# Optimization experiments

Hardware: AMD Instinct MI355X
Metric: run time of the kernel (lower is better)

Reference implementation:

```python
import jax, jax.numpy as jnp
import numpy as np
import math

HEAD_DIM = 128
N_HEADS_Q = 32
N_KV_HEADS = 8
N_REP = N_HEADS_Q // N_KV_HEADS
ROPE_BASE = 10000.0


def _rope(x, start_pos):
    # x: [b, s, h, d] -- rotate interleaved pairs, Llama-style
    b, s, h, d = x.shape
    pos = start_pos + jnp.arange(s, dtype=jnp.float32)            # [s]
    inv_freq = 1.0 / (ROPE_BASE ** (jnp.arange(0, d, 2, dtype=jnp.float32) / d))  # [d/2]
    ang = pos[:, None] * inv_freq[None, :]                         # [s, d/2]
    cos = jnp.cos(ang)[None, :, None, :].astype(x.dtype)
    sin = jnp.sin(ang)[None, :, None, :].astype(x.dtype)
    x1 = x[..., 0::2]
    x2 = x[..., 1::2]
    out = jnp.stack([x1 * cos - x2 * sin, x1 * sin + x2 * cos], axis=-1)
    return out.reshape(b, s, h, d)


def setup_inputs() -> dict:
    key = jax.random.key(0)
    ks = jax.random.split(key, 5)
    dim = N_HEADS_Q * HEAD_DIM
    kv_dim = N_KV_HEADS * HEAD_DIM
    sc = 0.02
    return {
        "x": jax.random.normal(ks[0], (2, 2048, dim), dtype=jnp.float32),
        "wq": jax.random.normal(ks[1], (dim, dim), dtype=jnp.float32) * sc,
        "wk": jax.random.normal(ks[2], (kv_dim, dim), dtype=jnp.float32) * sc,
        "wv": jax.random.normal(ks[3], (kv_dim, dim), dtype=jnp.float32) * sc,
        "wo": jax.random.normal(ks[4], (dim, dim), dtype=jnp.float32) * sc,
        "start_pos": 0,
    }


def reference(x, wq, wk, wv, wo, start_pos):
    b, s, dim = x.shape
    # QKV projections (nn.Linear: y = x @ W.T)
    xq = (x @ wq.T).reshape(b, s, N_HEADS_Q, HEAD_DIM)
    xk = (x @ wk.T).reshape(b, s, N_KV_HEADS, HEAD_DIM)
    xv = (x @ wv.T).reshape(b, s, N_KV_HEADS, HEAD_DIM)
    xq = _rope(xq, start_pos)
    xk = _rope(xk, start_pos)
    # KV cache: start_pos=0 prefill -> cached prefix == freshly written xk/xv
    keys, values = xk, xv
    # GQA attention without materializing repeated KV:
    # q grouped as [b, q, n_kv, n_rep, d]
    qg = xq.reshape(b, s, N_KV_HEADS, N_REP, HEAD_DIM)
    scores = jnp.einsum("bqhrd,bkhd->bhrqk", qg, keys) / math.sqrt(HEAD_DIM)
    probs = jax.nn.softmax(scores, axis=-1)  # no causal mask in original
    out = jnp.einsum("bhrqk,bkhd->bqhrd", probs, values)
    out = out.reshape(b, s, N_HEADS_Q * HEAD_DIM)
    return out @ wo.T
```

## Files before the change

kernel.cpp:

```cpp
#include <hip/hip_runtime.h>
#include <cstdint>
#include <cstddef>

typedef _Float16 f16x8 __attribute__((ext_vector_type(8)));
typedef _Float16 f16x4 __attribute__((ext_vector_type(4)));
typedef _Float16 f16x2 __attribute__((ext_vector_type(2)));
typedef float    f32x4 __attribute__((ext_vector_type(4)));
typedef uint32_t u32x4 __attribute__((ext_vector_type(4)));

__device__ __forceinline__ void async16(const void* g, void* l) {
  __builtin_amdgcn_global_load_lds(
      (const __attribute__((address_space(1))) void*)g,
      (__attribute__((address_space(3))) void*)l, 16, 0, 0);
}

__global__ void cvt5_kernel(const float* __restrict__ s0, const float* __restrict__ s1,
                            const float* __restrict__ s2, const float* __restrict__ s3,
                            const float* __restrict__ s4,
                            _Float16* __restrict__ d0, _Float16* __restrict__ d1,
                            _Float16* __restrict__ d2, _Float16* __restrict__ d3,
                            _Float16* __restrict__ d4,
                            int n0, int n1, int n2, int n3, int n4c) {
  const float* src; _Float16* dst; int n4;
  switch (blockIdx.y) {
    case 0:  src = s0; dst = d0; n4 = n0;  break;
    case 1:  src = s1; dst = d1; n4 = n1;  break;
    case 2:  src = s2; dst = d2; n4 = n2;  break;
    case 3:  src = s3; dst = d3; n4 = n3;  break;
    default: src = s4; dst = d4; n4 = n4c; break;
  }
  int i = blockIdx.x * blockDim.x + threadIdx.x;
  int stride = gridDim.x * blockDim.x;
  for (; i < n4; i += stride) {
    float4 f = ((const float4*)src)[i];
    f16x4 o;
    o[0] = (_Float16)f.x; o[1] = (_Float16)f.y;
    o[2] = (_Float16)f.z; o[3] = (_Float16)f.w;
    ((f16x4*)dst)[i] = o;
  }
}

__global__ void rope2_kernel(_Float16* __restrict__ XQ, _Float16* __restrict__ XK,
                             const int* __restrict__ sp, int sMask,
                             int nPairsQ, int nPairsK) {
  _Float16* X; int ppShift, nPairs;
  if (blockIdx.y == 0) { X = XQ; ppShift = 11; nPairs = nPairsQ; }
  else                 { X = XK; ppShift = 9;  nPairs = nPairsK; }
  int i = blockIdx.x * blockDim.x + threadIdx.x;
  int stride = gridDim.x * blockDim.x;
  int start = *sp;
  for (int p = i; p < nPairs; p += stride) {
    int row = p >> ppShift;
    int pc  = p & ((1 << ppShift) - 1);
    int fi  = pc & 63;
    int s   = row & sMask;
    float ang = (float)(start + s) * exp2f(-0.20762050593046014f * (float)fi);
    float sn, cs;
    __sincosf(ang, &sn, &cs);
    uint32_t u = ((uint32_t*)X)[p];
    f16x2 v = __builtin_bit_cast(f16x2, u);
    float x1 = (float)v[0], x2 = (float)v[1];
    v[0] = (_Float16)(x1 * cs - x2 * sn);
    v[1] = (_Float16)(x1 * sn + x2 * cs);
    ((uint32_t*)X)[p] = __builtin_bit_cast(uint32_t, v);
  }
}

template<int OUT_MODE>
__global__ __launch_bounds__(256, 3)
void gemm_nt(const _Float16* __restrict__ A, const _Float16* __restrict__ B,
             void* __restrict__ Cp, void* __restrict__ Cp2, void* __restrict__ Cp3,
             int M, int N, int K) {
  __shared__ __align__(16) _Float16 As[128 * 64];
  __shared__ __align__(16) _Float16 Bs[128 * 64];
  const int tid  = threadIdx.x;
  const int wave = tid >> 6, lane = tid & 63;
  const int l15  = lane & 15, quad = lane >> 4;
  const int m0 = blockIdx.y * 128, n0 = blockIdx.x * 128;
  const int wm = (wave >> 1) * 64, wn = (wave & 1) * 64;
  f32x4 acc[4][4] = {};
  const int cbase = wave * 256;

  for (int kb = 0; kb < K; kb += 64) {
    #pragma unroll
    for (int i = 0; i < 4; ++i) {
      int base = cbase + i * 64;
      int idx  = base + lane;
      int row  = idx >> 3, pos = idx & 7;
      int c    = pos ^ (row & 7);
      async16(A + (size_t)(m0 + row) * K + kb + c * 8, (char*)As + base * 16);
      async16(B + (size_t)(n0 + row) * K + kb + c * 8, (char*)Bs + base * 16);
    }
    __syncthreads();
    #pragma unroll
    for (int ks = 0; ks < 2; ++ks) {
      f16x8 af[4], bfv[4];
      #pragma unroll
      for (int t = 0; t < 4; ++t) {
        int ra = wm + t * 16 + l15;
        int pa = (ks * 4 + quad) ^ (ra & 7);
        af[t] = *(const f16x8*)((const char*)As + ra * 128 + pa * 16);
        int rb = wn + t * 16 + l15;
        int pb = (ks * 4 + quad) ^ (rb & 7);
        bfv[t] = *(const f16x8*)((const char*)Bs + rb * 128 + pb * 16);
      }
      #pragma unroll
      for (int mt = 0; mt < 4; ++mt)
        #pragma unroll
        for (int nt = 0; nt < 4; ++nt)
          acc[mt][nt] = __builtin_amdgcn_mfma_f32_16x16x32_f16(af[mt], bfv[nt], acc[mt][nt], 0, 0, 0);
    }
    __syncthreads();
  }

  if constexpr (OUT_MODE == 2) {
    float* Cf = (float*)Cp;
    #pragma unroll
    for (int mt = 0; mt < 4; ++mt)
      #pragma unroll
      for (int r = 0; r < 4; ++r) {
        size_t row = (size_t)(m0 + wm + mt * 16 + quad * 4 + r);
        #pragma unroll
        for (int nt = 0; nt < 4; ++nt)
          Cf[row * N + n0 + wn + nt * 16 + l15] = acc[mt][nt][r];
      }
  } else if constexpr (OUT_MODE == 4) {
    if (n0 < 4096) {
      _Float16* Cb = (_Float16*)Cp;
      #pragma unroll
      for (int mt = 0; mt < 4; ++mt)
        #pragma unroll
        for (int r = 0; r < 4; ++r) {
          size_t row = (size_t)(m0 + wm + mt * 16 + quad * 4 + r);
          #pragma unroll
          for (int nt = 0; nt < 4; ++nt)
            Cb[row * 4096 + n0 + wn + nt * 16 + l15] = (_Float16)acc[mt][nt][r];
        }
    } else if (n0 < 5120) {
      _Float16* Cb = (_Float16*)Cp2;
      #pragma unroll
      for (int mt = 0; mt < 4; ++mt)
        #pragma unroll
        for (int r = 0; r < 4; ++r) {
          size_t row = (size_t)(m0 + wm + mt * 16 + quad * 4 + r);
          #pragma unroll
          for (int nt = 0; nt < 4; ++nt)
            Cb[row * 1024 + (n0 - 4096) + wn + nt * 16 + l15] = (_Float16)acc[mt][nt][r];
        }
    } else {
      _Float16* Ct = (_Float16*)Cp3;
      #pragma unroll
      for (int mt = 0; mt < 4; ++mt)
        #pragma unroll
        for (int nt = 0; nt < 4; ++nt) {
          size_t crow = (size_t)(n0 - 5120 + wn + nt * 16 + l15);
          size_t ccol = (size_t)(m0 + wm + mt * 16 + quad * 4);
          f16x4 t;
          t[0] = (_Float16)acc[mt][nt][0]; t[1] = (_Float16)acc[mt][nt][1];
          t[2] = (_Float16)acc[mt][nt][2]; t[3] = (_Float16)acc[mt][nt][3];
          *(f16x4*)(Ct + crow * M + ccol) = t;
        }
    }
  }
}

__global__ __launch_bounds__(256, 2)
void flash_kernel(const _Float16* __restrict__ Q, const _Float16* __restrict__ Kg,
                  const _Float16* __restrict__ Vt, _Float16* __restrict__ O,
                  int S, int T) {
  __shared__ __align__(16) _Float16 Kt[64 * 128];
  __shared__ __align__(16) _Float16 Vs[128 * 64];
  const int tid  = threadIdx.x;
  const int wave = tid >> 6, lane = tid & 63;
  const int l15  = lane & 15, quad = lane >> 4;
  const int qt = blockIdx.x, hq = blockIdx.y, b = blockIdx.z;
  const int kvh = hq >> 2;
  const float scale = 0.12751744f;

  f16x8 qf[2][4];
  #pragma unroll
  for (int mt = 0; mt < 2; ++mt)
    #pragma unroll
    for (int ks = 0; ks < 4; ++ks) {
      size_t row = (size_t)b * S + qt * 128 + wave * 32 + mt * 16 + l15;
      qf[mt][ks] = *(const f16x8*)(Q + row * 4096 + hq * 128 + ks * 32 + quad * 8);
    }

  const f16x8 ones = {(_Float16)1, (_Float16)1, (_Float16)1, (_Float16)1,
                      (_Float16)1, (_Float16)1, (_Float16)1, (_Float16)1};

  f32x4 oacc[2][8] = {};
  f32x4 liacc[2] = {};
  float mi[2] = {-1e30f, -1e30f};

  const int nkt = S >> 6;

  auto stageK = [&](int kt) {
    #pragma unroll
    for (int i = 0; i < 4; ++i) {
      int base = wave * 256 + i * 64;
      int idx  = base + lane;
      int row = idx >> 4, pos = idx & 15, c = pos ^ (row & 15);
      async16(Kg + (size_t)(b * S + kt * 64 + row) * 1024 + kvh * 128 + c * 8,
              (char*)Kt + base * 16);
    }
  };
  auto stageV = [&](int kt) {
    #pragma unroll
    for (int i = 0; i < 4; ++i) {
      int base = wave * 256 + i * 64;
      int idx  = base + lane;
      int row = idx >> 3, pos = idx & 7, c = pos ^ (row & 7);
      async16(Vt + (size_t)(kvh * 128 + row) * T + b * S + kt * 64 + c * 8,
              (char*)Vs + base * 16);
    }
  };

  stageK(0); stageV(0);
  __syncthreads();

  const int idxA = l15 + (((quad * 2) & 3) << 4);
  const int idxB = l15 + (((quad * 2 + 1) & 3) << 4);
  const bool hiNt = (quad >> 1) != 0;

  for (int kt = 0; kt < nkt; ++kt) {
    f32x4 sacc[2][4] = {};
    #pragma unroll
    for (int ks = 0; ks < 4; ++ks) {
      f16x8 kf[4];
      #pragma unroll
      for (int nt = 0; nt < 4; ++nt) {
        int rk = nt * 16 + l15;
        int pp = (ks * 4 + quad) ^ (rk & 15);
        kf[nt] = *(const f16x8*)((const char*)Kt + rk * 256 + pp * 16);
      }
      __builtin_amdgcn_s_setprio(1);
      #pragma unroll
      for (int mt = 0; mt < 2; ++mt)
        #pragma unroll
        for (int nt = 0; nt < 4; ++nt)
          sacc[mt][nt] = __builtin_amdgcn_mfma_f32_16x16x32_f16(kf[nt], qf[mt][ks], sacc[mt][nt], 0, 0, 0);
      __builtin_amdgcn_s_setprio(0);
    }

    __syncthreads();
    if (kt + 1 < nkt) stageK(kt + 1);

    f16x8 pf[2][2];
    #pragma unroll
    for (int mt = 0; mt < 2; ++mt) {
      float a0 = fmaxf(fmaxf(sacc[mt][0][0], sacc[mt][0][1]), fmaxf(sacc[mt][0][2], sacc[mt][0][3]));
      float a1 = fmaxf(fmaxf(sacc[mt][1][0], sacc[mt][1][1]), fmaxf(sacc[mt][1][2], sacc[mt][1][3]));
      float a2 = fmaxf(fmaxf(sacc[mt][2][0], sacc[mt][2][1]), fmaxf(sacc[mt][2][2], sacc[mt][2][3]));
      float a3 = fmaxf(fmaxf(sacc[mt][3][0], sacc[mt][3][1]), fmaxf(sacc[mt][3][2], sacc[mt][3][3]));
      float mx = fmaxf(fmaxf(a0, a1), fmaxf(a2, a3));
      mx = fmaxf(mx, __shfl_xor(mx, 16));
      mx = fmaxf(mx, __shfl_xor(mx, 32));
      if (__any(mx > mi[mt] + 24.0f)) {
        float mnew = fmaxf(mi[mt], mx);
        float al = exp2f((mi[mt] - mnew) * scale);
        mi[mt] = mnew;
        #pragma unroll
        for (int r = 0; r < 4; ++r) {
          float alr = __shfl(al, quad * 4 + r);
          liacc[mt][r] *= alr;
          #pragma unroll
          for (int nt = 0; nt < 8; ++nt) oacc[mt][nt][r] *= alr;
        }
      }
      float nm = -mi[mt] * scale;
      #pragma unroll
      for (int nt = 0; nt < 4; ++nt)
        #pragma unroll
        for (int r = 0; r < 4; ++r)
          sacc[mt][nt][r] = exp2f(fmaf(sacc[mt][nt][r], scale, nm));
      uint32_t pd[4][2];
      #pragma unroll
      for (int nt = 0; nt < 4; ++nt) {
        f16x2 lo2, hi2;
        lo2[0] = (_Float16)sacc[mt][nt][0]; lo2[1] = (_Float16)sacc[mt][nt][1];
        hi2[0] = (_Float16)sacc[mt][nt][2]; hi2[1] = (_Float16)sacc[mt][nt][3];
        pd[nt][0] = __builtin_bit_cast(uint32_t, lo2);
        pd[nt][1] = __builtin_bit_cast(uint32_t, hi2);
      }
      #pragma unroll
      for (int k2 = 0; k2 < 2; ++k2) {
        uint32_t w[4];
        #pragma unroll
        for (int h = 0; h < 2; ++h) {
          uint32_t a0v = (uint32_t)__shfl((int)pd[2 * k2][h],     idxA);
          uint32_t a1v = (uint32_t)__shfl((int)pd[2 * k2 + 1][h], idxA);
          w[h] = hiNt ? a1v : a0v;
          uint32_t b0v = (uint32_t)__shfl((int)pd[2 * k2][h],     idxB);
          uint32_t b1v = (uint32_t)__shfl((int)pd[2 * k2 + 1][h], idxB);
          w[2 + h] = hiNt ? b1v : b0v;
        }
        u32x4 wv = {w[0], w[1], w[2], w[3]};
        pf[mt][k2] = __builtin_bit_cast(f16x8, wv);
      }
    }

    #pragma unroll
    for (int k2 = 0; k2 < 2; ++k2) {
      f16x8 vf[8];
      #pragma unroll
      for (int nt = 0; nt < 8; ++nt) {
        int rv = nt * 16 + l15;
        int pv = (k2 * 4 + quad) ^ (rv & 7);
        vf[nt] = *(const f16x8*)((const char*)Vs + rv * 128 + pv * 16);
      }
      __builtin_amdgcn_s_setprio(1);
      #pragma unroll
      for (int mt = 0; mt < 2; ++mt)
        liacc[mt] = __builtin_amdgcn_mfma_f32_16x16x32_f16(pf[mt][k2], ones, liacc[mt], 0, 0, 0);
      #pragma unroll
      for (int mt = 0; mt < 2; ++mt)
        #pragma unroll
        for (int nt = 0; nt < 8; ++nt)
          oacc[mt][nt] = __builtin_amdgcn_mfma_f32_16x16x32_f16(pf[mt][k2], vf[nt], oacc[mt][nt], 0, 0, 0);
      __builtin_amdgcn_s_setprio(0);
    }

    __syncthreads();
    if (kt + 1 < nkt) stageV(kt + 1);
  }

  #pragma unroll
  for (int mt = 0; mt < 2; ++mt)
    #pragma unroll
    for (int r = 0; r < 4; ++r) {
      float inv = 1.0f / liacc[mt][r];
      size_t row = (size_t)b * S + qt * 128 + wave * 32 + mt * 16 + quad * 4 + r;
      #pragma unroll
      for (int nt = 0; nt < 8; ++nt)
        O[row * 4096 + hq * 128 + nt * 16 + l15] = (_Float16)(oacc[mt][nt][r] * inv);
    }
}

extern "C" void kernel_launch(void* const* d_in, const int* in_sizes, int n_in,
                              void* d_out, int out_size, void* d_ws, size_t ws_size,
                              hipStream_t stream) {
  const float* x  = (const float*)d_in[0];
  const float* wq = (const float*)d_in[1];
  const float* wk = (const float*)d_in[2];
  const float* wv = (const float*)d_in[3];
  const float* wo = (const float*)d_in[4];
  const int*   sp = (const int*)d_in[5];

  const int dim = 4096, kvdim = 1024;
  const int T = in_sizes[0] / dim;
  const int B = 2;
  const int S = T / B;

  _Float16* xb   = (_Float16*)d_ws;
  _Float16* wqb  = xb   + (size_t)T * dim;
  _Float16* wkvb = wqb  + (size_t)dim * dim;
  _Float16* wob  = wkvb + (size_t)2 * kvdim * dim;
  _Float16* XQ   = wob  + (size_t)dim * dim;
  _Float16* XK   = XQ   + (size_t)T * dim;
  _Float16* VT   = XK   + (size_t)T * kvdim;
  _Float16* AO   = xb;

  cvt5_kernel<<<dim3(2048, 5), 256, 0, stream>>>(
      x, wq, wk, wv, wo,
      xb, wqb, wkvb, wkvb + (size_t)kvdim * dim, wob,
      (int)((size_t)T * dim / 4), (int)((size_t)dim * dim / 4),
      (int)((size_t)kvdim * dim / 4), (int)((size_t)kvdim * dim / 4),
      (int)((size_t)dim * dim / 4));

  gemm_nt<4><<<dim3((dim + 2 * kvdim) / 128, T / 128), 256, 0, stream>>>(
      xb, wqb, XQ, XK, VT, T, dim + 2 * kvdim, dim);

  rope2_kernel<<<dim3(4096, 2), 256, 0, stream>>>(
      XQ, XK, sp, S - 1, (int)((size_t)T * dim / 2), (int)((size_t)T * kvdim / 2));

  flash_kernel<<<dim3(S / 128, 32, B), 256, 0, stream>>>(XQ, XK, VT, AO, S, T);

  gemm_nt<2><<<dim3(dim / 128, T / 128), 256, 0, stream>>>(AO, wob, d_out, nullptr, nullptr, T, dim, dim);
}
```

Before: 762.9 us.

## Fuse RoPE into QKV GEMM epilogue and restructure flash P·V loop

```diff
diff --git a/kernel.cpp b/kernel.cpp
--- a/kernel.cpp
+++ b/kernel.cpp
@@ -40,37 +40,12 @@
   }
 }
 
-__global__ void rope2_kernel(_Float16* __restrict__ XQ, _Float16* __restrict__ XK,
-                             const int* __restrict__ sp, int sMask,
-                             int nPairsQ, int nPairsK) {
-  _Float16* X; int ppShift, nPairs;
-  if (blockIdx.y == 0) { X = XQ; ppShift = 11; nPairs = nPairsQ; }
-  else                 { X = XK; ppShift = 9;  nPairs = nPairsK; }
-  int i = blockIdx.x * blockDim.x + threadIdx.x;
-  int stride = gridDim.x * blockDim.x;
-  int start = *sp;
-  for (int p = i; p < nPairs; p += stride) {
-    int row = p >> ppShift;
-    int pc  = p & ((1 << ppShift) - 1);
-    int fi  = pc & 63;
-    int s   = row & sMask;
-    float ang = (float)(start + s) * exp2f(-0.20762050593046014f * (float)fi);
-    float sn, cs;
-    __sincosf(ang, &sn, &cs);
-    uint32_t u = ((uint32_t*)X)[p];
-    f16x2 v = __builtin_bit_cast(f16x2, u);
-    float x1 = (float)v[0], x2 = (float)v[1];
-    v[0] = (_Float16)(x1 * cs - x2 * sn);
-    v[1] = (_Float16)(x1 * sn + x2 * cs);
-    ((uint32_t*)X)[p] = __builtin_bit_cast(uint32_t, v);
-  }
-}
-
-template<int OUT_MODE>
-__global__ __launch_bounds__(256, 3)
+template<int OUT_MODE, int MINW>
+__global__ __launch_bounds__(256, MINW)
 void gemm_nt(const _Float16* __restrict__ A, const _Float16* __restrict__ B,
              void* __restrict__ Cp, void* __restrict__ Cp2, void* __restrict__ Cp3,
-             int M, int N, int K) {
+             const int* __restrict__ sp,
+             int M, int N, int K, int sMask) {
   __shared__ __align__(16) _Float16 As[128 * 64];
   __shared__ __align__(16) _Float16 Bs[128 * 64];
   const int tid  = threadIdx.x;
@@ -125,27 +100,32 @@
           Cf[row * N + n0 + wn + nt * 16 + l15] = acc[mt][nt][r];
       }
   } else if constexpr (OUT_MODE == 4) {
-    if (n0 < 4096) {
-      _Float16* Cb = (_Float16*)Cp;
+    if (n0 < 5120) {
+      const bool isQ = (n0 < 4096);
+      _Float16* Cb = isQ ? (_Float16*)Cp : (_Float16*)Cp2;
+      const int ld   = isQ ? 4096 : 1024;
+      const int cof  = isQ ? 0 : 4096;
+      const int start = *sp;
+      const bool odd = (l15 & 1) != 0;
       #pragma unroll
       for (int mt = 0; mt < 4; ++mt)
         #pragma unroll
         for (int r = 0; r < 4; ++r) {
-          size_t row = (size_t)(m0 + wm + mt * 16 + quad * 4 + r);
+          int row = m0 + wm + mt * 16 + quad * 4 + r;
+          float pos = (float)(start + (row & sMask));
           #pragma unroll
-          for (int nt = 0; nt < 4; ++nt)
-            Cb[row * 4096 + n0 + wn + nt * 16 + l15] = (_Float16)acc[mt][nt][r];
-        }
-    } else if (n0 < 5120) {
-      _Float16* Cb = (_Float16*)Cp2;
-      #pragma unroll
-      for (int mt = 0; mt < 4; ++mt)
-        #pragma unroll
-        for (int r = 0; r < 4; ++r) {
-          size_t row = (size_t)(m0 + wm + mt * 16 + quad * 4 + r);
-          #pragma unroll
-          for (int nt = 0; nt < 4; ++nt)
-            Cb[row * 1024 + (n0 - 4096) + wn + nt * 16 + l15] = (_Float16)acc[mt][nt][r];
+          for (int nt = 0; nt < 4; ++nt) {
+            int col = n0 - cof + wn + nt * 16 + l15;
+            int fi  = (col & 127) >> 1;
+            float ang = pos * exp2f(-0.20762050593046014f * (float)fi);
+            float sn, cs;
+            __sincosf(ang, &sn, &cs);
+            float self  = acc[mt][nt][r];
+            float other = __shfl_xor(self, 1);
+            float out = odd ? (other * sn + self * cs)
+                            : (self * cs - other * sn);
+            Cb[(size_t)row * ld + col] = (_Float16)out;
+          }
         }
     } else {
       _Float16* Ct = (_Float16*)Cp3;
@@ -246,7 +226,6 @@
     __syncthreads();
     if (kt + 1 < nkt) stageK(kt + 1);
 
-    f16x8 pf[2][2];
     #pragma unroll
     for (int mt = 0; mt < 2; ++mt) {
       float a0 = fmaxf(fmaxf(sacc[mt][0][0], sacc[mt][0][1]), fmaxf(sacc[mt][0][2], sacc[mt][0][3]));
@@ -283,6 +262,7 @@
         pd[nt][0] = __builtin_bit_cast(uint32_t, lo2);
         pd[nt][1] = __builtin_bit_cast(uint32_t, hi2);
       }
+      f16x8 pfk[2];
       #pragma unroll
       for (int k2 = 0; k2 < 2; ++k2) {
         uint32_t w[4];
@@ -296,29 +276,24 @@
           w[2 + h] = hiNt ? b1v : b0v;
         }
         u32x4 wv = {w[0], w[1], w[2], w[3]};
-        pf[mt][k2] = __builtin_bit_cast(f16x8, wv);
-      }
-    }
-
-    #pragma unroll
-    for (int k2 = 0; k2 < 2; ++k2) {
-      f16x8 vf[8];
-      #pragma unroll
-      for (int nt = 0; nt < 8; ++nt) {
-        int rv = nt * 16 + l15;
-        int pv = (k2 * 4 + quad) ^ (rv & 7);
-        vf[nt] = *(const f16x8*)((const char*)Vs + rv * 128 + pv * 16);
-      }
-      __builtin_amdgcn_s_setprio(1);
-      #pragma unroll
-      for (int mt = 0; mt < 2; ++mt)
-        liacc[mt] = __builtin_amdgcn_mfma_f32_16x16x32_f16(pf[mt][k2], ones, liacc[mt], 0, 0, 0);
-      #pragma unroll
-      for (int mt = 0; mt < 2; ++mt)
+        pfk[k2] = __builtin_bit_cast(f16x8, wv);
+      }
+      #pragma unroll
+      for (int k2 = 0; k2 < 2; ++k2) {
+        f16x8 vf[8];
+        #pragma unroll
+        for (int nt = 0; nt < 8; ++nt) {
+          int rv = nt * 16 + l15;
+          int pv = (k2 * 4 + quad) ^ (rv & 7);
+          vf[nt] = *(const f16x8*)((const char*)Vs + rv * 128 + pv * 16);
+        }
+        __builtin_amdgcn_s_setprio(1);
+        liacc[mt] = __builtin_amdgcn_mfma_f32_16x16x32_f16(pfk[k2], ones, liacc[mt], 0, 0, 0);
         #pragma unroll
         for (int nt = 0; nt < 8; ++nt)
-          oacc[mt][nt] = __builtin_amdgcn_mfma_f32_16x16x32_f16(pf[mt][k2], vf[nt], oacc[mt][nt], 0, 0, 0);
-      __builtin_amdgcn_s_setprio(0);
+          oacc[mt][nt] = __builtin_amdgcn_mfma_f32_16x16x32_f16(pfk[k2], vf[nt], oacc[mt][nt], 0, 0, 0);
+        __builtin_amdgcn_s_setprio(0);
+      }
     }
 
     __syncthreads();
@@ -368,13 +343,11 @@
       (int)((size_t)kvdim * dim / 4), (int)((size_t)kvdim * dim / 4),
       (int)((size_t)dim * dim / 4));
 
-  gemm_nt<4><<<dim3((dim + 2 * kvdim) / 128, T / 128), 256, 0, stream>>>(
-      xb, wqb, XQ, XK, VT, T, dim + 2 * kvdim, dim);
-
-  rope2_kernel<<<dim3(4096, 2), 256, 0, stream>>>(
-      XQ, XK, sp, S - 1, (int)((size_t)T * dim / 2), (int)((size_t)T * kvdim / 2));
+  gemm_nt<4, 3><<<dim3((dim + 2 * kvdim) / 128, T / 128), 256, 0, stream>>>(
+      xb, wqb, XQ, XK, VT, sp, T, dim + 2 * kvdim, dim, S - 1);
 
   flash_kernel<<<dim3(S / 128, 32, B), 256, 0, stream>>>(XQ, XK, VT, AO, S, T);
 
-  gemm_nt<2><<<dim3(dim / 128, T / 128), 256, 0, stream>>>(AO, wob, d_out, nullptr, nullptr, T, dim, dim);
-}
+  gemm_nt<2, 4><<<dim3(dim / 128, T / 128), 256, 0, stream>>>(
+      AO, wob, d_out, nullptr, nullptr, nullptr, T, dim, dim, 0);
+}
```

Result: slower. 839.3 us (+10.0%).
